# Performance work log

Hardware: AMD Instinct MI355X
Metric: run time of the kernel (lower is better)

## Reference

```python
import jax, jax.numpy as jnp
import numpy as np

K_SEL = 16  # number of selected positions per distribution
EPS = 1e-20


def setup_inputs() -> dict:
    key = jax.random.key(0)
    k1, k2 = jax.random.split(key)
    d0, vocab, BS = 64, 2048, 32
    logits = jax.random.normal(k1, (d0, vocab), dtype=jnp.float32)
    # Gumbel noise exactly as in the dense branch: -0.001*log(-log(U+eps)+eps)
    u = jax.random.uniform(k2, (BS, d0, vocab), dtype=jnp.float32)
    gn = -0.001 * jnp.log(-jnp.log(u + EPS) + EPS)
    return {"logits": logits, "gn": gn}


def reference(logits, gn):
    # logits: [d0, V], gn: [BS, d0, V]
    vocab = logits.shape[-1]
    perturbed = logits[None, :, :] + gn                     # [BS, d0, V]
    # top-k indices of perturbed logits, then top-k of the indices themselves
    # (sorts the selected indices descending); reverse -> ascending order.
    _, idx = jax.lax.top_k(perturbed, K_SEL)                # [BS, d0, k]
    idx_sorted, _ = jax.lax.top_k(idx, K_SEL)               # descending indices
    topk = idx_sorted[..., ::-1]                            # ascending
    hard = jax.nn.one_hot(topk, vocab, dtype=logits.dtype)  # [BS, d0, k, V]
    # exclusive cumsum mask along the k axis
    cum_mask = jnp.cumsum(hard, axis=-2) - hard             # [BS, d0, k, V]
    Temp = 1.0
    prob_exp = jnp.exp(logits)[None, :, None, :]            # [1, d0, 1, V]
    soft = jax.nn.sigmoid(
        (jnp.log(prob_exp * (1.0 - cum_mask + EPS)) + gn[:, :, None, :]) / Temp
    )                                                        # [BS, d0, k, V]
    return jax.lax.stop_gradient(hard - soft) + soft
```

## Files before the change

### kernel.cpp

```cpp
#include <hip/hip_runtime.h>
#include <math.h>

#define K_SEL   16
#define VOCAB   2048
#define NROWS   2048

__global__ __launch_bounds__(64) void topk_onehot_kernel(
    const float* __restrict__ logits,
    const float* __restrict__ gn,
    float* __restrict__ out)
{
    const int row  = blockIdx.x;
    const int d0   = row & 63;
    const int lane = threadIdx.x;

    const float* grow = gn     + (size_t)row * VOCAB;
    const float* lrow = logits + (size_t)d0  * VOCAB;
    float*       orow = out    + (size_t)row * (K_SEL * VOCAB);

    float v[32];
    #pragma unroll
    for (int seg = 0; seg < 8; ++seg) {
        const int c = seg * 256 + lane * 4;
        const float4 g = *reinterpret_cast<const float4*>(grow + c);
        const float4 l = *reinterpret_cast<const float4*>(lrow + c);
        v[seg * 4 + 0] = l.x + g.x;
        v[seg * 4 + 1] = l.y + g.y;
        v[seg * 4 + 2] = l.z + g.z;
        v[seg * 4 + 3] = l.w + g.w;
    }

    float lv = v[0]; int ls = 0;
    #pragma unroll
    for (int i = 1; i < 32; ++i) { if (v[i] > lv) { lv = v[i]; ls = i; } }

    int sel[K_SEL];

    #pragma unroll
    for (int k = 0; k < K_SEL; ++k) {
        float bv = lv;
        int   bc = ((ls >> 2) << 8) + lane * 4 + (ls & 3);
        #pragma unroll
        for (int off = 1; off < 64; off <<= 1) {
            const float ov = __shfl_xor(bv, off);
            const int   oc = __shfl_xor(bc, off);
            if (ov > bv || (ov == bv && oc < bc)) { bv = ov; bc = oc; }
        }
        sel[k] = bc;
        if (lane == ((bc >> 2) & 63)) {
            const int s = (((bc >> 8) & 7) << 2) | (bc & 3);
            lv = -INFINITY; ls = 0;
            #pragma unroll
            for (int i = 0; i < 32; ++i) {
                if (i == s) v[i] = -INFINITY;
                if (v[i] > lv) { lv = v[i]; ls = i; }
            }
        }
    }

    #pragma unroll
    for (int k = 0; k < K_SEL; ++k) {
        int r = 0;
        #pragma unroll
        for (int j = 0; j < K_SEL; ++j) r += (sel[j] < sel[k]) ? 1 : 0;
        const int one = sel[k];
        float* rbase = orow + (size_t)r * VOCAB;
        #pragma unroll
        for (int seg = 0; seg < 8; ++seg) {
            const int c = seg * 256 + lane * 4;
            float4 a;
            a.x = (c + 0 == one) ? 1.0f : 0.0f;
            a.y = (c + 1 == one) ? 1.0f : 0.0f;
            a.z = (c + 2 == one) ? 1.0f : 0.0f;
            a.w = (c + 3 == one) ? 1.0f : 0.0f;
            *reinterpret_cast<float4*>(rbase + c) = a;
        }
    }
}

extern "C" void kernel_launch(void* const* d_in, const int* in_sizes, int n_in,
                              void* d_out, int out_size, void* d_ws, size_t ws_size,
                              hipStream_t stream) {
    const float* logits = (const float*)d_in[0];
    const float* gn     = (const float*)d_in[1];
    float* out          = (float*)d_out;

    hipLaunchKernelGGL(topk_onehot_kernel, dim3(NROWS), dim3(64), 0, stream,
                       logits, gn, out);
}
```

Baseline: 59.83 us.

## Pack four rows per workgroup, share sorted indices via LDS, nontemporal stores

Each 256-thread workgroup now handles four rows, one wavefront per row for the top-k search. The sorted selected indices go through shared memory so all 256 threads can cooperatively write the 64 one-hot output rows with nontemporal vector stores. The goal is to cut launch and workgroup overhead and to make the output write stream, which dominates traffic, more efficient and avoid polluting the cache. In exchange it adds a block barrier and fewer, larger workgroups.

```diff
diff --git a/kernel.cpp b/kernel.cpp
--- a/kernel.cpp
+++ b/kernel.cpp
@@ -4,19 +4,27 @@
 #define K_SEL   16
 #define VOCAB   2048
 #define NROWS   2048
+#define RPW     4
+#define WGS     (NROWS / RPW)
 
-__global__ __launch_bounds__(64) void topk_onehot_kernel(
+typedef float vf4 __attribute__((ext_vector_type(4)));
+
+__global__ __launch_bounds__(256) void topk_onehot_fused(
     const float* __restrict__ logits,
     const float* __restrict__ gn,
     float* __restrict__ out)
 {
-    const int row  = blockIdx.x;
+    const int bid  = blockIdx.x;
+    const int tid  = threadIdx.x;
+    const int lane = tid & 63;
+    const int w    = tid >> 6;
+    const int row  = bid * RPW + w;
     const int d0   = row & 63;
-    const int lane = threadIdx.x;
+
+    __shared__ int onec[RPW][K_SEL];
 
     const float* grow = gn     + (size_t)row * VOCAB;
     const float* lrow = logits + (size_t)d0  * VOCAB;
-    float*       orow = out    + (size_t)row * (K_SEL * VOCAB);
 
     float v[32];
     #pragma unroll
@@ -35,7 +43,6 @@
     for (int i = 1; i < 32; ++i) { if (v[i] > lv) { lv = v[i]; ls = i; } }
 
     int sel[K_SEL];
-
     #pragma unroll
     for (int k = 0; k < K_SEL; ++k) {
         float bv = lv;
@@ -58,22 +65,34 @@
         }
     }
 
-    #pragma unroll
-    for (int k = 0; k < K_SEL; ++k) {
+    if (lane < K_SEL) {
+        int my = sel[0];
+        #pragma unroll
+        for (int k = 1; k < K_SEL; ++k) { if (lane == k) my = sel[k]; }
         int r = 0;
         #pragma unroll
-        for (int j = 0; j < K_SEL; ++j) r += (sel[j] < sel[k]) ? 1 : 0;
-        const int one = sel[k];
-        float* rbase = orow + (size_t)r * VOCAB;
+        for (int j = 0; j < K_SEL; ++j) r += (sel[j] < my) ? 1 : 0;
+        onec[w][r] = my;
+    }
+    __syncthreads();
+
+    float* obase = out + (size_t)bid * (RPW * K_SEL * VOCAB);
+    #pragma unroll
+    for (int r4 = 0; r4 < RPW; ++r4) {
         #pragma unroll
-        for (int seg = 0; seg < 8; ++seg) {
-            const int c = seg * 256 + lane * 4;
-            float4 a;
-            a.x = (c + 0 == one) ? 1.0f : 0.0f;
-            a.y = (c + 1 == one) ? 1.0f : 0.0f;
-            a.z = (c + 2 == one) ? 1.0f : 0.0f;
-            a.w = (c + 3 == one) ? 1.0f : 0.0f;
-            *reinterpret_cast<float4*>(rbase + c) = a;
+        for (int k = 0; k < K_SEL; ++k) {
+            const int one = onec[r4][k];
+            float* rbase = obase + ((r4 * K_SEL + k) * VOCAB);
+            #pragma unroll
+            for (int t = 0; t < 2; ++t) {
+                const int c = (t * 256 + tid) * 4;
+                vf4 a;
+                a.x = (c + 0 == one) ? 1.0f : 0.0f;
+                a.y = (c + 1 == one) ? 1.0f : 0.0f;
+                a.z = (c + 2 == one) ? 1.0f : 0.0f;
+                a.w = (c + 3 == one) ? 1.0f : 0.0f;
+                __builtin_nontemporal_store(a, reinterpret_cast<vf4*>(rbase + c));
+            }
         }
     }
 }
@@ -85,6 +104,6 @@
     const float* gn     = (const float*)d_in[1];
     float* out          = (float*)d_out;
 
-    hipLaunchKernelGGL(topk_onehot_kernel, dim3(NROWS), dim3(64), 0, stream,
+    hipLaunchKernelGGL(topk_onehot_fused, dim3(WGS), dim3(256), 0, stream,
                        logits, gn, out);
 }
```

New measurement: 71.74 us. 1.2x slower.
